# Performance work log

Measured on AMD Instinct MI355X. Metric: run time of the kernel, lower is better.

Reference implementation:

```python
import jax, jax.numpy as jnp
import numpy as np

N_NODES = 25000
N_EDGES = 250000
DIM = 64
HEADS = 4
BN_EPS = 1e-5


def setup_inputs() -> dict:
    key = jax.random.key(0)
    ks = jax.random.split(key, 6)
    x = jax.random.normal(ks[0], (N_NODES, DIM), dtype=jnp.float32)
    edge_index = jax.random.randint(ks[1], (2, N_EDGES), 0, N_NODES)
    edge_attr = jax.random.normal(ks[2], (N_EDGES, DIM), dtype=jnp.float32)
    # learned params of GATGNN_AGAT_LAYER (xavier-ish scale)
    W = jax.random.normal(ks[3], (2 * DIM, HEADS * DIM), dtype=jnp.float32) * 0.05
    att = jax.random.normal(ks[4], (1, HEADS, 2 * DIM), dtype=jnp.float32) * 0.05
    bias = jnp.zeros((DIM,), dtype=jnp.float32)
    # BatchNorm1d(heads) in eval mode (running stats)
    bn_gamma = jnp.ones((HEADS,), dtype=jnp.float32)
    bn_beta = jnp.zeros((HEADS,), dtype=jnp.float32)
    bn_mean = jnp.zeros((HEADS,), dtype=jnp.float32)
    bn_var = jnp.ones((HEADS,), dtype=jnp.float32)
    return {"x": x, "edge_attr": edge_attr, "W": W, "att": att, "bias": bias,
            "bn_gamma": bn_gamma, "bn_beta": bn_beta, "bn_mean": bn_mean,
            "bn_var": bn_var, "edge_index": edge_index}


def reference(x, edge_attr, W, att, bias, bn_gamma, bn_beta, bn_mean, bn_var, edge_index):
    act = jax.nn.softplus  # act='softplus' in DSDCrystal
    # flow='target_to_source': i = edge_index[0] (aggregation index), j = edge_index[1]
    idx_i = edge_index[0]
    idx_j = edge_index[1]
    x_i = x[idx_i]                                   # [E, D] gather
    x_j = x[idx_j]                                   # [E, D] gather
    out_i = act(jnp.concatenate([x_i, edge_attr], axis=-1) @ W)  # [E, H*D]
    out_j = act(jnp.concatenate([x_j, edge_attr], axis=-1) @ W)  # [E, H*D]
    out_i = out_i.reshape(-1, HEADS, DIM)            # [E, H, D]
    out_j = out_j.reshape(-1, HEADS, DIM)
    # multi-head attention logits
    alpha = act(jnp.sum(jnp.concatenate([out_i, out_j], axis=-1) * att, axis=-1))  # [E, H]
    # BatchNorm1d(heads), eval mode
    alpha = act((alpha - bn_mean) / jnp.sqrt(bn_var + BN_EPS) * bn_gamma + bn_beta)
    # segment softmax over edges sharing the same target node i
    amax = jax.ops.segment_max(alpha, idx_i, num_segments=N_NODES)  # [N, H]
    e = jnp.exp(alpha - amax[idx_i])
    denom = jax.ops.segment_sum(e, idx_i, num_segments=N_NODES)[idx_i]  # [E, H]
    alpha = e / denom
    # weighted messages, scatter-add aggregation (dropout p=0.0 / eval)
    msg = out_j * alpha[:, :, None]                  # [E, H, D]
    aggr = jax.ops.segment_sum(msg, idx_i, num_segments=N_NODES)  # [N, H, D]
    # update: mean over heads + bias
    return aggr.mean(axis=1) + bias                  # [N, D]
```

## Files before the change

kernel.cpp:

```cpp
#include <hip/hip_runtime.h>
#include <hip/hip_bf16.h>
#include <math.h>

#define NN 25000
#define NE 250000
#define DD 64
#define HH 4
#define NGROUP (NE / 16)

typedef __attribute__((ext_vector_type(8))) short bf16x8;
typedef __attribute__((ext_vector_type(4))) float f32x4;

#define WT_LD 136

__device__ __forceinline__ float softplus_f(float x) {
    return fmaxf(x, 0.0f) + __logf(1.0f + __expf(-fabsf(x)));
}

__device__ __forceinline__ unsigned short f2bf(float f) {
    __hip_bfloat16 h = __float2bfloat16(f);
    unsigned short u;
    __builtin_memcpy(&u, &h, 2);
    return u;
}

__device__ __forceinline__ float bf2f(unsigned short u) {
    return __uint_as_float(((unsigned int)u) << 16);
}

__device__ __forceinline__ void load8(const float* p, bf16x8& hi, bf16x8& lo) {
    float4 a = *(const float4*)p;
    float4 b = *(const float4*)(p + 4);
    float v[8] = {a.x, a.y, a.z, a.w, b.x, b.y, b.z, b.w};
#pragma unroll
    for (int i = 0; i < 8; ++i) {
        unsigned short h = f2bf(v[i]);
        hi[i] = (short)h;
        lo[i] = (short)f2bf(v[i] - bf2f(h));
    }
}

__global__ __launch_bounds__(1024, 2)
void k_edge(const float* __restrict__ x, const float* __restrict__ ea,
            const float* __restrict__ W, const float* __restrict__ att,
            const float* __restrict__ bn_g, const float* __restrict__ bn_b,
            const float* __restrict__ bn_m, const float* __restrict__ bn_v,
            const int* __restrict__ eidx,
            unsigned short* __restrict__ outj,
            float* __restrict__ expa)
{
    __shared__ unsigned short Wsh[256 * WT_LD];
    __shared__ float attI[256], attJ[256];

    const int tid = threadIdx.x;
    const int lane = tid & 63;
    const int q = lane >> 4;
    const int r = lane & 15;

    for (int idx = tid; idx < 32768; idx += 1024) {
        int k = idx >> 8, n = idx & 255;
        Wsh[n * WT_LD + k] = f2bf(W[idx]);
    }
    if (tid < 256) {
        int c = tid;
        attI[c] = att[(c >> 6) * 128 + (c & 63)];
        attJ[c] = att[(c >> 6) * 128 + 64 + (c & 63)];
    }
    float bnsc[HH], bnsh[HH];
#pragma unroll
    for (int t = 0; t < HH; ++t) {
        float inv = rsqrtf(bn_v[t] + 1e-5f);
        bnsc[t] = bn_g[t] * inv;
        bnsh[t] = bn_b[t] - bn_m[t] * bn_g[t] * inv;
    }
    __syncthreads();

    const int gw = blockIdx.x * 16 + (tid >> 6);
    const int nw = gridDim.x * 16;

    for (int g = gw; g < NGROUP; g += nw) {
        const int e0 = g * 16;
        const int ei = eidx[e0 + r];
        const int ej = eidx[NE + e0 + r];
        const float* xi = x + (size_t)ei * DD;
        const float* xj = x + (size_t)ej * DD;
        const float* ev = ea + (size_t)(e0 + r) * DD;

        bf16x8 Ahi[6], Alo[6];
        load8(xi + q * 8,      Ahi[0], Alo[0]);
        load8(xi + 32 + q * 8, Ahi[1], Alo[1]);
        load8(xj + q * 8,      Ahi[2], Alo[2]);
        load8(xj + 32 + q * 8, Ahi[3], Alo[3]);
        load8(ev + q * 8,      Ahi[4], Alo[4]);
        load8(ev + 32 + q * 8, Ahi[5], Alo[5]);

        float lg[4][4];
#pragma unroll
        for (int a = 0; a < 4; ++a)
#pragma unroll
            for (int b = 0; b < 4; ++b) lg[a][b] = 0.f;

#pragma unroll
        for (int nt = 0; nt < 4; ++nt) {
            f32x4 ai[4], aj[4];
#pragma unroll
            for (int h = 0; h < 4; ++h) {
                ai[h] = (f32x4){0.f, 0.f, 0.f, 0.f};
                aj[h] = (f32x4){0.f, 0.f, 0.f, 0.f};
            }
#pragma unroll
            for (int h = 0; h < 4; ++h) {
                const unsigned short* bp = &Wsh[((nt + 4 * h) * 16 + r) * WT_LD + q * 8];
#pragma unroll
                for (int kt = 0; kt < 4; ++kt) {
                    bf16x8 bf = *(const bf16x8*)(bp + kt * 32);
                    const int fi = (kt < 2) ? kt : kt + 2;
                    const int fj = kt + 2;
                    ai[h] = __builtin_amdgcn_mfma_f32_16x16x32_bf16(Ahi[fi], bf, ai[h], 0, 0, 0);
                    ai[h] = __builtin_amdgcn_mfma_f32_16x16x32_bf16(Alo[fi], bf, ai[h], 0, 0, 0);
                    aj[h] = __builtin_amdgcn_mfma_f32_16x16x32_bf16(Ahi[fj], bf, aj[h], 0, 0, 0);
                    aj[h] = __builtin_amdgcn_mfma_f32_16x16x32_bf16(Alo[fj], bf, aj[h], 0, 0, 0);
                }
            }
            const int dbase = nt * 16 + r;
#pragma unroll
            for (int reg = 0; reg < 4; ++reg) {
                ushort4 pk;
                unsigned short* pkp = (unsigned short*)&pk;
#pragma unroll
                for (int h = 0; h < 4; ++h) {
                    const int c = dbase + 64 * h;
                    float spi = softplus_f(ai[h][reg]);
                    float spj = softplus_f(aj[h][reg]);
                    lg[reg][h] += spi * attI[c] + spj * attJ[c];
                    pkp[h] = f2bf(spj);
                }
                const unsigned e = (unsigned)(e0 + q * 4 + reg);
                *(ushort4*)&outj[e * 256 + dbase * 4] = pk;
            }
        }

#pragma unroll
        for (int off = 1; off < 16; off <<= 1) {
#pragma unroll
            for (int a = 0; a < 4; ++a)
#pragma unroll
                for (int b = 0; b < 4; ++b)
                    lg[a][b] += __shfl_xor(lg[a][b], off, 64);
        }
        float exv[4][4];
#pragma unroll
        for (int reg = 0; reg < 4; ++reg)
#pragma unroll
            for (int h = 0; h < 4; ++h)
                exv[reg][h] = __expf(softplus_f(fmaf(lg[reg][h], bnsc[h], bnsh[h])));

        if (r < 4) {
#pragma unroll
            for (int reg = 0; reg < 4; ++reg) {
                const int e = e0 + q * 4 + reg;
                expa[e * 4 + r] = exv[reg][r];
            }
        }
    }
}

__global__ __launch_bounds__(256)
void k_hist(const int* __restrict__ eidx, int* __restrict__ deg)
{
    const int e = blockIdx.x * 256 + threadIdx.x;
    if (e < NE) atomicAdd(&deg[eidx[e]], 1);
}

__global__ __launch_bounds__(1024)
void k_scan(const int* __restrict__ deg, int* __restrict__ offs)
{
    __shared__ int sh[1024];
    const int t = threadIdx.x;
    const int base = t * 25;
    int s = 0;
#pragma unroll
    for (int k = 0; k < 25; ++k) {
        int idx = base + k;
        if (idx < NN) s += deg[idx];
    }
    sh[t] = s;
    __syncthreads();
    for (int off = 1; off < 1024; off <<= 1) {
        int v = (t >= off) ? sh[t - off] : 0;
        __syncthreads();
        sh[t] += v;
        __syncthreads();
    }
    int run = sh[t] - s;
#pragma unroll
    for (int k = 0; k < 25; ++k) {
        int idx = base + k;
        if (idx < NN) {
            offs[idx] = run;
            run += deg[idx];
        } else if (idx == NN) {
            offs[NN] = run;
        }
    }
}

__global__ __launch_bounds__(256)
void k_fill(const int* __restrict__ eidx, const int* __restrict__ offs,
            int* __restrict__ cursor, int* __restrict__ elist)
{
    const int e = blockIdx.x * 256 + threadIdx.x;
    if (e < NE) {
        const int i = eidx[e];
        const int p = atomicAdd(&cursor[i], 1);
        elist[offs[i] + p] = e;
    }
}

__global__ __launch_bounds__(256)
void k_aggr(const int* __restrict__ offs, const int* __restrict__ elist,
            const unsigned short* __restrict__ outj,
            const float* __restrict__ expa,
            const float* __restrict__ bias, float* __restrict__ out)
{
    const int n = blockIdx.x * 4 + (threadIdx.x >> 6);
    const int lane = threadIdx.x & 63;
    const int beg = offs[n];
    const int end = offs[n + 1];

    float4 s = make_float4(0.f, 0.f, 0.f, 0.f);
    for (int t = beg + lane; t < end; t += 64) {
        const int e = elist[t];
        float4 v = *(const float4*)&expa[e * 4];
        s.x += v.x; s.y += v.y; s.z += v.z; s.w += v.w;
    }
#pragma unroll
    for (int off = 32; off >= 1; off >>= 1) {
        s.x += __shfl_xor(s.x, off, 64);
        s.y += __shfl_xor(s.y, off, 64);
        s.z += __shfl_xor(s.z, off, 64);
        s.w += __shfl_xor(s.w, off, 64);
    }
    const float w0 = 0.25f / s.x, w1 = 0.25f / s.y;
    const float w2 = 0.25f / s.z, w3 = 0.25f / s.w;

    float sum = 0.f;
    for (int t = beg; t < end; ++t) {
        const int e = elist[t];
        float4 ev = *(const float4*)&expa[e * 4];
        ushort4 v = *(const ushort4*)&outj[((unsigned)e << 8) | (lane << 2)];
        sum += (ev.x * w0) * bf2f(v.x) + (ev.y * w1) * bf2f(v.y)
             + (ev.z * w2) * bf2f(v.z) + (ev.w * w3) * bf2f(v.w);
    }
    out[n * DD + lane] = sum + bias[lane];
}

extern "C" void kernel_launch(void* const* d_in, const int* in_sizes, int n_in,
                              void* d_out, int out_size, void* d_ws, size_t ws_size,
                              hipStream_t stream)
{
    (void)in_sizes; (void)n_in; (void)out_size; (void)ws_size;
    const float* x    = (const float*)d_in[0];
    const float* ea   = (const float*)d_in[1];
    const float* W    = (const float*)d_in[2];
    const float* att  = (const float*)d_in[3];
    const float* bias = (const float*)d_in[4];
    const float* bn_g = (const float*)d_in[5];
    const float* bn_b = (const float*)d_in[6];
    const float* bn_m = (const float*)d_in[7];
    const float* bn_v = (const float*)d_in[8];
    const int*   eidx = (const int*)d_in[9];
    float* out = (float*)d_out;

    char* ws = (char*)d_ws;
    unsigned short* outj = (unsigned short*)ws;
    float* expa  = (float*)(ws + 128000000ull);
    int*   deg    = (int*)(ws + 132000000ull);
    int*   cursor = (int*)(ws + 132100000ull);
    int*   offs   = (int*)(ws + 132200000ull);
    int*   elist  = (int*)(ws + 132300032ull);

    hipMemsetAsync(deg, 0, 200000, stream);

    k_hist<<<dim3((NE + 255) / 256), dim3(256), 0, stream>>>(eidx, deg);
    k_scan<<<dim3(1), dim3(1024), 0, stream>>>(deg, offs);
    k_fill<<<dim3((NE + 255) / 256), dim3(256), 0, stream>>>(eidx, offs, cursor, elist);
    k_edge<<<dim3(256), dim3(1024), 0, stream>>>(
        x, ea, W, att, bn_g, bn_b, bn_m, bn_v, eidx, outj, expa);
    k_aggr<<<dim3(NN / 4), dim3(256), 0, stream>>>(offs, elist, outj, expa, bias, out);
}
```

Before: 356.7 us.

## Simplify softmax math, fold BN scale, single-pass aggregation, cheaper bf16 packing

The BN scale is folded into the attention vectors, and exp(softplus(z)) is replaced by the exact identity 1+exp(z), which removes a log and an exp per logit. The hi/lo bf16 split now uses bit truncation, and outputs are packed with paired bf16 conversions. The aggregation kernel now makes one pass over each node's edges, four edges per iteration, accumulating numerator and denominator together instead of doing a separate shuffle-reduced denominator pass. The edge kernel grid is doubled to 512 blocks; 1+exp(z) could overflow for large logits.

```diff
diff --git a/kernel.cpp b/kernel.cpp
--- a/kernel.cpp
+++ b/kernel.cpp
@@ -34,9 +34,10 @@
     float v[8] = {a.x, a.y, a.z, a.w, b.x, b.y, b.z, b.w};
 #pragma unroll
     for (int i = 0; i < 8; ++i) {
-        unsigned short h = f2bf(v[i]);
-        hi[i] = (short)h;
-        lo[i] = (short)f2bf(v[i] - bf2f(h));
+        unsigned int u = __float_as_uint(v[i]);
+        hi[i] = (short)(u >> 16);
+        float hf = __uint_as_float(u & 0xffff0000u);
+        lo[i] = (short)(__float_as_uint(v[i] - hf) >> 16);
     }
 }
 
@@ -57,21 +58,23 @@
     const int q = lane >> 4;
     const int r = lane & 15;
 
-    for (int idx = tid; idx < 32768; idx += 1024) {
-        int k = idx >> 8, n = idx & 255;
-        Wsh[n * WT_LD + k] = f2bf(W[idx]);
-    }
-    if (tid < 256) {
-        int c = tid;
-        attI[c] = att[(c >> 6) * 128 + (c & 63)];
-        attJ[c] = att[(c >> 6) * 128 + 64 + (c & 63)];
-    }
     float bnsc[HH], bnsh[HH];
 #pragma unroll
     for (int t = 0; t < HH; ++t) {
         float inv = rsqrtf(bn_v[t] + 1e-5f);
         bnsc[t] = bn_g[t] * inv;
         bnsh[t] = bn_b[t] - bn_m[t] * bn_g[t] * inv;
+    }
+
+    for (int idx = tid; idx < 32768; idx += 1024) {
+        int k = idx >> 8, n = idx & 255;
+        Wsh[n * WT_LD + k] = f2bf(W[idx]);
+    }
+    if (tid < 256) {
+        int c = tid;
+        float sc = bnsc[c >> 6];
+        attI[c] = att[(c >> 6) * 128 + (c & 63)] * sc;
+        attJ[c] = att[(c >> 6) * 128 + 64 + (c & 63)] * sc;
     }
     __syncthreads();
 
@@ -125,18 +128,22 @@
             const int dbase = nt * 16 + r;
 #pragma unroll
             for (int reg = 0; reg < 4; ++reg) {
-                ushort4 pk;
-                unsigned short* pkp = (unsigned short*)&pk;
+                float sp[4];
 #pragma unroll
                 for (int h = 0; h < 4; ++h) {
                     const int c = dbase + 64 * h;
                     float spi = softplus_f(ai[h][reg]);
                     float spj = softplus_f(aj[h][reg]);
                     lg[reg][h] += spi * attI[c] + spj * attJ[c];
-                    pkp[h] = f2bf(spj);
+                    sp[h] = spj;
                 }
+                __hip_bfloat162 p01 = __float22bfloat162_rn(float2{sp[0], sp[1]});
+                __hip_bfloat162 p23 = __float22bfloat162_rn(float2{sp[2], sp[3]});
+                uint2 pk;
+                __builtin_memcpy(&pk.x, &p01, 4);
+                __builtin_memcpy(&pk.y, &p23, 4);
                 const unsigned e = (unsigned)(e0 + q * 4 + reg);
-                *(ushort4*)&outj[e * 256 + dbase * 4] = pk;
+                *(uint2*)&outj[e * 256 + dbase * 4] = pk;
             }
         }
 
@@ -153,7 +160,7 @@
         for (int reg = 0; reg < 4; ++reg)
 #pragma unroll
             for (int h = 0; h < 4; ++h)
-                exv[reg][h] = __expf(softplus_f(fmaf(lg[reg][h], bnsc[h], bnsh[h])));
+                exv[reg][h] = 1.0f + __expf(lg[reg][h] + bnsh[h]);
 
         if (r < 4) {
 #pragma unroll
@@ -228,31 +235,45 @@
     const int beg = offs[n];
     const int end = offs[n + 1];
 
-    float4 s = make_float4(0.f, 0.f, 0.f, 0.f);
-    for (int t = beg + lane; t < end; t += 64) {
+    float a0 = 0.f, a1 = 0.f, a2 = 0.f, a3 = 0.f;
+    float d0 = 0.f, d1 = 0.f, d2 = 0.f, d3 = 0.f;
+    int t = beg;
+    for (; t + 4 <= end; t += 4) {
+        const int e0 = elist[t], e1 = elist[t + 1];
+        const int e2 = elist[t + 2], e3 = elist[t + 3];
+        float4 x0 = *(const float4*)&expa[e0 * 4];
+        float4 x1 = *(const float4*)&expa[e1 * 4];
+        float4 x2 = *(const float4*)&expa[e2 * 4];
+        float4 x3 = *(const float4*)&expa[e3 * 4];
+        ushort4 v0 = *(const ushort4*)&outj[((unsigned)e0 << 8) | (lane << 2)];
+        ushort4 v1 = *(const ushort4*)&outj[((unsigned)e1 << 8) | (lane << 2)];
+        ushort4 v2 = *(const ushort4*)&outj[((unsigned)e2 << 8) | (lane << 2)];
+        ushort4 v3 = *(const ushort4*)&outj[((unsigned)e3 << 8) | (lane << 2)];
+        a0 += x0.x * bf2f(v0.x); a1 += x0.y * bf2f(v0.y);
+        a2 += x0.z * bf2f(v0.z); a3 += x0.w * bf2f(v0.w);
+        d0 += x0.x; d1 += x0.y; d2 += x0.z; d3 += x0.w;
+        a0 += x1.x * bf2f(v1.x); a1 += x1.y * bf2f(v1.y);
+        a2 += x1.z * bf2f(v1.z); a3 += x1.w * bf2f(v1.w);
+        d0 += x1.x; d1 += x1.y; d2 += x1.z; d3 += x1.w;
+        a0 += x2.x * bf2f(v2.x); a1 += x2.y * bf2f(v2.y);
+        a2 += x2.z * bf2f(v2.z); a3 += x2.w * bf2f(v2.w);
+        d0 += x2.x; d1 += x2.y; d2 += x2.z; d3 += x2.w;
+        a0 += x3.x * bf2f(v3.x); a1 += x3.y * bf2f(v3.y);
+        a2 += x3.z * bf2f(v3.z); a3 += x3.w * bf2f(v3.w);
+        d0 += x3.x; d1 += x3.y; d2 += x3.z; d3 += x3.w;
+    }
+    for (; t < end; ++t) {
         const int e = elist[t];
-        float4 v = *(const float4*)&expa[e * 4];
-        s.x += v.x; s.y += v.y; s.z += v.z; s.w += v.w;
-    }
-#pragma unroll
-    for (int off = 32; off >= 1; off >>= 1) {
-        s.x += __shfl_xor(s.x, off, 64);
-        s.y += __shfl_xor(s.y, off, 64);
-        s.z += __shfl_xor(s.z, off, 64);
-        s.w += __shfl_xor(s.w, off, 64);
-    }
-    const float w0 = 0.25f / s.x, w1 = 0.25f / s.y;
-    const float w2 = 0.25f / s.z, w3 = 0.25f / s.w;
-
-    float sum = 0.f;
-    for (int t = beg; t < end; ++t) {
-        const int e = elist[t];
-        float4 ev = *(const float4*)&expa[e * 4];
+        float4 xv = *(const float4*)&expa[e * 4];
         ushort4 v = *(const ushort4*)&outj[((unsigned)e << 8) | (lane << 2)];
-        sum += (ev.x * w0) * bf2f(v.x) + (ev.y * w1) * bf2f(v.y)
-             + (ev.z * w2) * bf2f(v.z) + (ev.w * w3) * bf2f(v.w);
-    }
-    out[n * DD + lane] = sum + bias[lane];
+        a0 += xv.x * bf2f(v.x); a1 += xv.y * bf2f(v.y);
+        a2 += xv.z * bf2f(v.z); a3 += xv.w * bf2f(v.w);
+        d0 += xv.x; d1 += xv.y; d2 += xv.z; d3 += xv.w;
+    }
+    float rsum = 0.f;
+    if (end > beg)
+        rsum = 0.25f * (a0 / d0 + a1 / d1 + a2 / d2 + a3 / d3);
+    out[n * DD + lane] = rsum + bias[lane];
 }
 
 extern "C" void kernel_launch(void* const* d_in, const int* in_sizes, int n_in,
@@ -285,7 +306,7 @@
     k_hist<<<dim3((NE + 255) / 256), dim3(256), 0, stream>>>(eidx, deg);
     k_scan<<<dim3(1), dim3(1024), 0, stream>>>(deg, offs);
     k_fill<<<dim3((NE + 255) / 256), dim3(256), 0, stream>>>(eidx, offs, cursor, elist);
-    k_edge<<<dim3(256), dim3(1024), 0, stream>>>(
+    k_edge<<<dim3(512), dim3(1024), 0, stream>>>(
         x, ea, W, att, bn_g, bn_b, bn_m, bn_v, eidx, outj, expa);
     k_aggr<<<dim3(NN / 4), dim3(256), 0, stream>>>(offs, elist, outj, expa, bias, out);
 }
```

Result: slower. 825.7 us (+131.5%).
